# Performance work log

Measured on AMD Instinct MI355X. Metric: run time of the kernel, lower is better.

## Reference

```python
import jax, jax.numpy as jnp
import numpy as np

N_NODES = 100_000
N_EDGES = 1_600_000
B = 2
CH_N = 8; CH_E = 8; CH_K = 8; HID = 16
DT = 1.0
MAX_VALUE = 1e6


def _mlp(x, w1, b1, w2, b2):
    return jnp.tanh(x @ w1 + b1) @ w2 + b2


def _soft_clamp(x):
    return MAX_VALUE * jnp.tanh(x / MAX_VALUE)


def _seg_attn(logit, msg, seg, n):
    # logit [E], msg [E,C]; softmax over edges sharing a segment, weighted sum.
    mx = jax.ops.segment_max(logit, seg, num_segments=n)
    ex = jnp.exp(logit - mx[seg])
    den = jax.ops.segment_sum(ex, seg, num_segments=n)
    num = jax.ops.segment_sum(ex[:, None] * msg, seg, num_segments=n)
    return num / (den[:, None] + 1e-10)


def setup_inputs() -> dict:
    key = jax.random.key(0)
    ks = jax.random.split(key, 20)
    r = lambda k, shp, sc=0.3: (jax.random.normal(k, shp, dtype=jnp.float32) * sc)
    inp = {
        "nodes": jax.random.normal(ks[0], (B, N_NODES, CH_N), dtype=jnp.float32),
        "edges": jax.random.normal(ks[1], (B, N_EDGES, CH_E), dtype=jnp.float32),
        "msg_w1": r(ks[2], (2 * CH_N + CH_E, HID)),
        "msg_b1": jnp.zeros((HID,), jnp.float32),
        "msg_w2": r(ks[3], (HID, 2 * CH_N + CH_E)),
        "msg_b2": jnp.zeros((2 * CH_N + CH_E,), jnp.float32),
        "att_w1": r(ks[4], (CH_N, HID)),
        "att_b1": jnp.zeros((HID,), jnp.float32),
        "att_w2": r(ks[5], (HID, 4 * CH_K)),
        "att_b2": jnp.zeros((4 * CH_K,), jnp.float32),
        "upd_w1": r(ks[6], (3 * CH_N, HID)),
        "upd_b1": jnp.zeros((HID,), jnp.float32),
        "upd_w2": r(ks[7], (HID, CH_N)),
        "upd_b2": jnp.zeros((CH_N,), jnp.float32),
        "sources": jax.random.randint(ks[8], (N_EDGES,), 0, N_NODES, dtype=jnp.int32).astype(jnp.int64) if False else jax.random.randint(ks[8], (N_EDGES,), 0, N_NODES),
        "targets": jax.random.randint(ks[9], (N_EDGES,), 0, N_NODES),
    }
    return inp


def reference(nodes, edges, msg_w1, msg_b1, msg_w2, msg_b2,
              att_w1, att_b1, att_w2, att_b2,
              upd_w1, upd_b1, upd_w2, upd_b2,
              sources, targets):
    # --- per-edge messages: gather endpoint nodes, concat with edge state ---
    m_x = jnp.concatenate([nodes[:, sources], nodes[:, targets], edges], axis=2)  # [B,E,2*ch_n+ch_e]
    m = _mlp(m_x, msg_w1, msg_b1, msg_w2, msg_b2)
    m_a = m[..., :CH_N]                 # message to source node
    m_b = m[..., CH_N:2 * CH_N]         # message to target node
    m_ab = m[..., 2 * CH_N:]            # edge update

    # --- attention keys/queries per node (4*ch_k) ---
    att = _mlp(nodes, att_w1, att_b1, att_w2, att_b2)  # [B,N,4*ch_k]
    a_key, a_query, b_key, b_query = jnp.split(att, 4, axis=2)
    scale = 1.0 / np.sqrt(CH_K).astype(np.float32)
    logit_a = (a_query[:, sources] * b_key[:, targets]).sum(-1) * scale  # [B,E]
    logit_b = (b_query[:, targets] * a_key[:, sources]).sum(-1) * scale

    agg_a = jax.vmap(lambda l, ms: _seg_attn(l, ms, sources, N_NODES))(logit_a, m_a)  # [B,N,ch_n]
    agg_b = jax.vmap(lambda l, ms: _seg_attn(l, ms, targets, N_NODES))(logit_b, m_b)

    # --- node update ---
    u_x = jnp.concatenate([nodes, agg_a, agg_b], axis=2)  # [B,N,3*ch_n]
    upd = _mlp(u_x, upd_w1, upd_b1, upd_w2, upd_b2)

    new_nodes = _soft_clamp(nodes + DT * upd)
    new_edges = _soft_clamp(edges + DT * m_ab)
    return new_nodes, new_edges
```

## Files before the change

### kernel.cpp

```cpp
#include <hip/hip_runtime.h>

#define NN 100000
#define NE 1600000
#define NB 2
#define CH 8
#define HID 16
#define NTILES 98

typedef unsigned int uint;
typedef float f32x4 __attribute__((ext_vector_type(4)));

__device__ __forceinline__ float soft_clamp(float x) {
    float y = x * 1e-6f;
    return x * (1.0f - 0.33333333f * y * y);
}
__device__ __forceinline__ float fast_tanh(float x) {
    float ax = fabsf(x);
    float t = __expf(-2.0f * ax);
    float r = (1.0f - t) / (1.0f + t);
    return copysignf(r, x);
}
__device__ __forceinline__ void load8(const float* __restrict__ p, float* x) {
    float4 a = ((const float4*)p)[0];
    float4 b = ((const float4*)p)[1];
    x[0]=a.x; x[1]=a.y; x[2]=a.z; x[3]=a.w; x[4]=b.x; x[5]=b.y; x[6]=b.z; x[7]=b.w;
}
__device__ __forceinline__ void store8(float* __restrict__ p, const float* x) {
    ((float4*)p)[0] = make_float4(x[0],x[1],x[2],x[3]);
    ((float4*)p)[1] = make_float4(x[4],x[5],x[6],x[7]);
}
__device__ __forceinline__ void f4w(float* p, float4 v){ p[0]=v.x; p[1]=v.y; p[2]=v.z; p[3]=v.w; }

__device__ __forceinline__ uint bfu(float x) {
    uint u = __float_as_uint(x);
    return (u + 0x7fffu + ((u >> 16) & 1u)) >> 16;
}
__device__ __forceinline__ float ubf(uint u) { return __uint_as_float(u << 16); }

__device__ __forceinline__ ushort f2h(float x) {
    _Float16 h = (_Float16)x;
    union { _Float16 h; ushort u; } c; c.h = h; return c.u;
}
__device__ __forceinline__ float h2f(uint u) {
    union { ushort u; _Float16 h; } c; c.u = (ushort)u; return (float)c.h;
}
__device__ __forceinline__ float dot8h(uint4 a, uint4 b) {
    const uint* pa = &a.x; const uint* pb = &b.x;
    float s = 0.0f;
#pragma unroll
    for (int i = 0; i < 4; i++) {
        s += h2f(pa[i] & 0xffffu) * h2f(pb[i] & 0xffffu);
        s += h2f(pa[i] >> 16)     * h2f(pb[i] >> 16);
    }
    return s;
}

__device__ __forceinline__ void acc8(float* h, uint4 v, const float* __restrict__ w) {
    const uint* p = &v.x;
#pragma unroll
    for (int i = 0; i < 4; i++) {
        float x0 = h2f(p[i] & 0xffffu), x1 = h2f(p[i] >> 16);
#pragma unroll
        for (int j = 0; j < HID; j++) h[j] += x0 * w[(2*i)*HID + j];
#pragma unroll
        for (int j = 0; j < HID; j++) h[j] += x1 * w[(2*i+1)*HID + j];
    }
}

__device__ __forceinline__ void dot_pair(const float* __restrict__ h,
                                         const float* __restrict__ sw2,
                                         const float* __restrict__ sb2,
                                         int kp, float& a0, float& a1) {
    a0 = sb2[2*kp]; a1 = sb2[2*kp+1];
#pragma unroll
    for (int j = 0; j < HID; j++) {
        a0 += h[j] * sw2[j*24 + 2*kp];
        a1 += h[j] * sw2[j*24 + 2*kp + 1];
    }
}

__global__ void __launch_bounds__(256)
att_pack_kernel(const float* __restrict__ nodes,
                const float* __restrict__ w1, const float* __restrict__ b1,
                const float* __restrict__ w2, const float* __restrict__ b2,
                uint4* __restrict__ S, uint4* __restrict__ T,
                float4* __restrict__ nodesP,
                int* __restrict__ cntA, int* __restrict__ cntB) {
    __shared__ float sw1[CH*HID], sb1[HID], sw2[HID*32], sb2[32];
    int tid = threadIdx.x;
    for (int i = tid; i < CH*HID; i += 256) sw1[i] = w1[i];
    for (int i = tid; i < HID; i += 256) sb1[i] = b1[i];
    for (int i = tid; i < HID*32; i += 256) sw2[i] = w2[i];
    for (int i = tid; i < 32; i += 256) sb2[i] = b2[i];
    __syncthreads();
    int n = blockIdx.x * 256 + tid;
    if (n >= NN) return;
    int b = blockIdx.y;
    size_t base = (size_t)b * NN + n;

    if (b == 0) { cntA[n] = 0; cntB[n] = 0; }

    float x[CH];
    load8(nodes + base * CH, x);
    nodesP[(size_t)n*4 + b*2]     = make_float4(x[0],x[1],x[2],x[3]);
    nodesP[(size_t)n*4 + b*2 + 1] = make_float4(x[4],x[5],x[6],x[7]);

    float h[HID];
#pragma unroll
    for (int j = 0; j < HID; j++) {
        float acc = sb1[j];
#pragma unroll
        for (int i = 0; i < CH; i++) acc += x[i] * sw1[i*HID + j];
        h[j] = fast_tanh(acc);
    }
    float o[32];
#pragma unroll
    for (int k = 0; k < 32; k++) {
        float acc = sb2[k];
#pragma unroll
        for (int j = 0; j < HID; j++) acc += h[j] * sw2[j*32 + k];
        o[k] = acc;
    }
    uint4 nx, ak, aq, bk, bq;
    nx.x=f2h(x[0]) |(f2h(x[1]) <<16); nx.y=f2h(x[2]) |(f2h(x[3]) <<16);
    nx.z=f2h(x[4]) |(f2h(x[5]) <<16); nx.w=f2h(x[6]) |(f2h(x[7]) <<16);
    ak.x=f2h(o[0]) |(f2h(o[1]) <<16); ak.y=f2h(o[2]) |(f2h(o[3]) <<16);
    ak.z=f2h(o[4]) |(f2h(o[5]) <<16); ak.w=f2h(o[6]) |(f2h(o[7]) <<16);
    aq.x=f2h(o[8]) |(f2h(o[9]) <<16); aq.y=f2h(o[10])|(f2h(o[11])<<16);
    aq.z=f2h(o[12])|(f2h(o[13])<<16); aq.w=f2h(o[14])|(f2h(o[15])<<16);
    bk.x=f2h(o[16])|(f2h(o[17])<<16); bk.y=f2h(o[18])|(f2h(o[19])<<16);
    bk.z=f2h(o[20])|(f2h(o[21])<<16); bk.w=f2h(o[22])|(f2h(o[23])<<16);
    bq.x=f2h(o[24])|(f2h(o[25])<<16); bq.y=f2h(o[26])|(f2h(o[27])<<16);
    bq.z=f2h(o[28])|(f2h(o[29])<<16); bq.w=f2h(o[30])|(f2h(o[31])<<16);
    size_t sl = (size_t)n*8 + b*4;
    S[sl+0] = nx; S[sl+1] = ak; S[sl+2] = aq;
    T[sl+0] = nx; T[sl+1] = bk; T[sl+2] = bq;
}

__global__ void __launch_bounds__(256)
hist_rank_kernel(const int* __restrict__ src, const int* __restrict__ tgt,
                 int* __restrict__ cntA, int* __restrict__ cntB,
                 int* __restrict__ rankA, int* __restrict__ rankB) {
    int e = blockIdx.x * 256 + threadIdx.x;
    if (e >= NE) return;
    rankA[e] = atomicAdd(&cntA[src[e]], 1);
    rankB[e] = atomicAdd(&cntB[tgt[e]], 1);
}

__global__ void __launch_bounds__(256)
scan_part_kernel(const int* __restrict__ cnt, int* __restrict__ part) {
    int y = blockIdx.y;
    const int* c = cnt + (size_t)y * NN;
    __shared__ int s[256];
    int t = threadIdx.x, bx = blockIdx.x;
    int base = bx * 1024 + t * 4;
    int sum = 0;
#pragma unroll
    for (int k = 0; k < 4; k++) { int i = base + k; sum += (i < NN) ? c[i] : 0; }
    s[t] = sum; __syncthreads();
    for (int off = 128; off > 0; off >>= 1) { if (t < off) s[t] += s[t + off]; __syncthreads(); }
    if (t == 0) part[y * 256 + bx] = s[0];
}

__global__ void __launch_bounds__(256)
scan_top_kernel(int* __restrict__ part, int* __restrict__ rowA, int* __restrict__ rowB) {
    int y = blockIdx.y; int t = threadIdx.x;
    __shared__ int s[256];
    int v = (t < NTILES) ? part[y * 256 + t] : 0;
    s[t] = v; __syncthreads();
    for (int off = 1; off < 256; off <<= 1) {
        int x = (t >= off) ? s[t - off] : 0;
        __syncthreads();
        s[t] += x;
        __syncthreads();
    }
    part[y * 256 + t] = t ? s[t - 1] : 0;
    if (t == 0) (y ? rowB : rowA)[NN] = NE;
}

__global__ void __launch_bounds__(256)
scan_down_kernel(const int* __restrict__ cnt, const int* __restrict__ part,
                 int* __restrict__ rowA, int* __restrict__ rowB) {
    int y = blockIdx.y;
    const int* c = cnt + (size_t)y * NN;
    int* row = y ? rowB : rowA;
    __shared__ int s[256];
    int t = threadIdx.x, bx = blockIdx.x;
    int base = bx * 1024 + t * 4;
    int v[4]; int tsum = 0;
#pragma unroll
    for (int k = 0; k < 4; k++) { int i = base + k; v[k] = (i < NN) ? c[i] : 0; tsum += v[k]; }
    s[t] = tsum; __syncthreads();
    for (int off = 1; off < 256; off <<= 1) {
        int x = (t >= off) ? s[t - off] : 0;
        __syncthreads();
        s[t] += x;
        __syncthreads();
    }
    int run = part[y * 256 + bx] + s[t] - tsum;
#pragma unroll
    for (int k = 0; k < 4; k++) {
        int i = base + k;
        if (i < NN) row[i] = run;
        run += v[k];
    }
}

__global__ void __launch_bounds__(256)
fill_kernel(const int* __restrict__ src, const int* __restrict__ tgt,
            const int* __restrict__ rowA, const int* __restrict__ rowB,
            const int* __restrict__ rankA, const int* __restrict__ rankB,
            int* __restrict__ eidA, int* __restrict__ eidB) {
    int e = blockIdx.x * 256 + threadIdx.x;
    if (e >= NE) return;
    eidA[rowA[src[e]] + rankA[e]] = e;
    eidB[rowB[tgt[e]] + rankB[e]] = e;
}

__global__ void __launch_bounds__(256, 2)
edge_kernel(const uint4* __restrict__ S, const uint4* __restrict__ T,
            const float* __restrict__ edges,
            const int* __restrict__ src, const int* __restrict__ tgt,
            const float* __restrict__ w1, const float* __restrict__ b1,
            const float* __restrict__ w2, const float* __restrict__ b2,
            float* __restrict__ out_edges,
            uint4* __restrict__ recA, uint4* __restrict__ recB) {
    __shared__ float sw1[24*HID], sb1[HID], sw2[HID*24], sb2[24];
    int tid = threadIdx.x;
    for (int i = tid; i < 24*HID; i += 256) sw1[i] = w1[i];
    for (int i = tid; i < HID; i += 256) sb1[i] = b1[i];
    for (int i = tid; i < HID*24; i += 256) sw2[i] = w2[i];
    for (int i = tid; i < 24; i += 256) sb2[i] = b2[i];
    __syncthreads();
    int b = blockIdx.x;
    int e = blockIdx.y * 256 + tid;
    int s = src[e], t = tgt[e];
    const float scale = 0.35355339059327373f;

    size_t sl = (size_t)s*8 + b*4, tl = (size_t)t*8 + b*4;
    uint4 sn = S[sl], ak = S[sl+1], aq = S[sl+2];
    uint4 tn = T[tl], bk = T[tl+1], bq = T[tl+2];
    f32x4 e0, e1;
    {
        const f32x4* ep = (const f32x4*)(edges + ((size_t)b*NE + e)*CH);
        e0 = __builtin_nontemporal_load(ep);
        e1 = __builtin_nontemporal_load(ep + 1);
    }

    float la = scale * dot8h(aq, bk);
    float lb = scale * dot8h(bq, ak);

    float h[HID];
#pragma unroll
    for (int j = 0; j < HID; j++) h[j] = sb1[j];
    acc8(h, sn, sw1);
    acc8(h, tn, sw1 + 8*HID);
    float ef[8];
    ef[0]=e0.x; ef[1]=e0.y; ef[2]=e0.z; ef[3]=e0.w;
    ef[4]=e1.x; ef[5]=e1.y; ef[6]=e1.z; ef[7]=e1.w;
#pragma unroll
    for (int i = 0; i < 8; i++) {
#pragma unroll
        for (int j = 0; j < HID; j++) h[j] += ef[i] * sw1[(16+i)*HID + j];
    }
#pragma unroll
    for (int j = 0; j < HID; j++) h[j] = fast_tanh(h[j]);

    uint wA[4], wB[4];
#pragma unroll
    for (int kp = 0; kp < 4; kp++) {
        float a0, a1;
        dot_pair(h, sw2, sb2, kp, a0, a1);
        wA[kp] = bfu(a0) | (bfu(a1) << 16);
    }
#pragma unroll
    for (int kp = 4; kp < 8; kp++) {
        float a0, a1;
        dot_pair(h, sw2, sb2, kp, a0, a1);
        wB[kp-4] = bfu(a0) | (bfu(a1) << 16);
    }
    f32x4 o0, o1;
    {
        float a0, a1;
        dot_pair(h, sw2, sb2, 8,  a0, a1); o0.x = soft_clamp(ef[0]+a0); o0.y = soft_clamp(ef[1]+a1);
        dot_pair(h, sw2, sb2, 9,  a0, a1); o0.z = soft_clamp(ef[2]+a0); o0.w = soft_clamp(ef[3]+a1);
        dot_pair(h, sw2, sb2, 10, a0, a1); o1.x = soft_clamp(ef[4]+a0); o1.y = soft_clamp(ef[5]+a1);
        dot_pair(h, sw2, sb2, 11, a0, a1); o1.z = soft_clamp(ef[6]+a0); o1.w = soft_clamp(ef[7]+a1);
    }

    {
        f32x4* op = (f32x4*)(out_edges + ((size_t)b*NE + e)*CH);
        __builtin_nontemporal_store(o0, op);
        __builtin_nontemporal_store(o1, op + 1);
    }

    recA[(size_t)e*4 + b*2]     = make_uint4(__float_as_uint(la), wA[0], wA[1], wA[2]);
    recA[(size_t)e*4 + b*2 + 1] = make_uint4(wA[3], 0u, 0u, 0u);
    recB[(size_t)e*4 + b*2]     = make_uint4(__float_as_uint(lb), wB[0], wB[1], wB[2]);
    recB[(size_t)e*4 + b*2 + 1] = make_uint4(wB[3], 0u, 0u, 0u);
}

__device__ __forceinline__ void aggregate1(int beg, int end, const int* __restrict__ eid,
                                           const uint4* __restrict__ rec, int boff,
                                           float* __restrict__ o) {
    float mx = -1e30f, den = 0.0f, num[CH];
#pragma unroll
    for (int c = 0; c < CH; c++) num[c] = 0.0f;
    for (int i = beg; i < end; ++i) {
        int e = eid[i];
        const uint4* P = rec + (size_t)e*4 + boff;
        uint4 q0 = P[0], q1 = P[1];
        float l = __uint_as_float(q0.x);
        float nm = fmaxf(mx, l);
        float r = __expf(mx - nm), w = __expf(l - nm);
        mx = nm; den = den * r + w;
        float mm[CH];
        mm[0]=ubf(q0.y&0xffffu); mm[1]=ubf(q0.y>>16);
        mm[2]=ubf(q0.z&0xffffu); mm[3]=ubf(q0.z>>16);
        mm[4]=ubf(q0.w&0xffffu); mm[5]=ubf(q0.w>>16);
        mm[6]=ubf(q1.x&0xffffu); mm[7]=ubf(q1.x>>16);
#pragma unroll
        for (int c = 0; c < CH; c++) num[c] = num[c] * r + w * mm[c];
    }
    float inv = 1.0f / (den + 1e-10f);
#pragma unroll
    for (int c = 0; c < CH; c++) o[c] = num[c] * inv;
}

__global__ void __launch_bounds__(256)
node_kernel(const float4* __restrict__ nodesP,
            const int* __restrict__ rowA, const int* __restrict__ rowB,
            const int* __restrict__ eidA, const int* __restrict__ eidB,
            const uint4* __restrict__ recA, const uint4* __restrict__ recB,
            const float* __restrict__ w1, const float* __restrict__ b1,
            const float* __restrict__ w2, const float* __restrict__ b2,
            float* __restrict__ out_nodes) {
    __shared__ float sw1[24*HID], sb1[HID], sw2[HID*CH], sb2[CH];
    int tid = threadIdx.x;
    for (int i = tid; i < 24*HID; i += 256) sw1[i] = w1[i];
    for (int i = tid; i < HID; i += 256) sb1[i] = b1[i];
    for (int i = tid; i < HID*CH; i += 256) sw2[i] = w2[i];
    for (int i = tid; i < CH; i += 256) sb2[i] = b2[i];
    __syncthreads();
    int g = blockIdx.x * 256 + tid;
    int n = g >> 1, b = g & 1;
    if (n >= NN) return;

    float in[24];
    float4 np0 = nodesP[(size_t)n*4 + b*2], np1 = nodesP[(size_t)n*4 + b*2 + 1];
    f4w(in, np0); f4w(in + 4, np1);

    aggregate1(rowA[n], rowA[n+1], eidA, recA, b*2, in + 8);
    aggregate1(rowB[n], rowB[n+1], eidB, recB, b*2, in + 16);

    float h[HID];
#pragma unroll
    for (int j = 0; j < HID; j++) {
        float acc = sb1[j];
#pragma unroll
        for (int i = 0; i < 24; i++) acc += in[i] * sw1[i*HID + j];
        h[j] = fast_tanh(acc);
    }
    float no[CH];
#pragma unroll
    for (int k = 0; k < CH; k++) {
        float acc = sb2[k];
#pragma unroll
        for (int j = 0; j < HID; j++) acc += h[j] * sw2[j*CH + k];
        no[k] = soft_clamp(in[k] + acc);
    }
    store8(out_nodes + ((size_t)b*NN + n)*CH, no);
}

extern "C" void kernel_launch(void* const* d_in, const int* in_sizes, int n_in,
                              void* d_out, int out_size, void* d_ws, size_t ws_size,
                              hipStream_t stream) {
    const float* nodes  = (const float*)d_in[0];
    const float* edges  = (const float*)d_in[1];
    const float* msg_w1 = (const float*)d_in[2];
    const float* msg_b1 = (const float*)d_in[3];
    const float* msg_w2 = (const float*)d_in[4];
    const float* msg_b2 = (const float*)d_in[5];
    const float* att_w1 = (const float*)d_in[6];
    const float* att_b1 = (const float*)d_in[7];
    const float* att_w2 = (const float*)d_in[8];
    const float* att_b2 = (const float*)d_in[9];
    const float* upd_w1 = (const float*)d_in[10];
    const float* upd_b1 = (const float*)d_in[11];
    const float* upd_w2 = (const float*)d_in[12];
    const float* upd_b2 = (const float*)d_in[13];
    const int*   sources = (const int*)d_in[14];
    const int*   targets = (const int*)d_in[15];

    float* out       = (float*)d_out;
    float* out_nodes = out;
    float* out_edges = out + (size_t)NB * NN * CH;

    char* wp = (char*)d_ws;
    size_t off = 0;
    auto take = [&](size_t bytes) -> char* {
        char* p = wp + off;
        off = (off + bytes + 255) & ~(size_t)255;
        return p;
    };
    uint4*  S      = (uint4*)take((size_t)NN * NB * 64);
    uint4*  T      = (uint4*)take((size_t)NN * NB * 64);
    float4* nodesP = (float4*)take((size_t)NN * 64);
    int*    cnt    = (int*)take((size_t)2 * NN * 4);
    int*    rowA   = (int*)take((size_t)(NN + 1) * 4);
    int*    rowB   = (int*)take((size_t)(NN + 1) * 4);
    int*    part   = (int*)take((size_t)2 * 256 * 4);
    int*    rankA  = (int*)take((size_t)NE * 4);
    int*    rankB  = (int*)take((size_t)NE * 4);
    int*    eidA   = (int*)take((size_t)NE * 4);
    int*    eidB   = (int*)take((size_t)NE * 4);
    uint4*  recA   = (uint4*)take((size_t)NE * 64);
    uint4*  recB   = (uint4*)take((size_t)NE * 64);
    int* cntA = cnt, *cntB = cnt + NN;

    dim3 gn((NN + 255) / 256, NB);
    dim3 gn2((2*NN + 255) / 256);
    dim3 ge1((NE + 255) / 256);
    dim3 geb(NB, NE / 256);
    dim3 gs(NTILES, 2);
    dim3 gt(1, 2);

    att_pack_kernel<<<gn, 256, 0, stream>>>(nodes, att_w1, att_b1, att_w2, att_b2,
                                            S, T, nodesP, cntA, cntB);
    hist_rank_kernel<<<ge1, 256, 0, stream>>>(sources, targets, cntA, cntB, rankA, rankB);
    scan_part_kernel<<<gs, 256, 0, stream>>>(cnt, part);
    scan_top_kernel<<<gt, 256, 0, stream>>>(part, rowA, rowB);
    scan_down_kernel<<<gs, 256, 0, stream>>>(cnt, part, rowA, rowB);
    fill_kernel<<<ge1, 256, 0, stream>>>(sources, targets, rowA, rowB, rankA, rankB,
                                         eidA, eidB);
    edge_kernel<<<geb, 256, 0, stream>>>(S, T, edges, sources, targets,
                                         msg_w1, msg_b1, msg_w2, msg_b2,
                                         out_edges, recA, recB);
    node_kernel<<<gn2, 256, 0, stream>>>(nodesP, rowA, rowB, eidA, eidB, recA, recB,
                                         upd_w1, upd_b1, upd_w2, upd_b2, out_nodes);
}
```

Baseline: 549.3 us.

## Process two edges per thread and interleave both node aggregation streams

The edge kernel now handles two edges per thread and issues all gather loads for both before computing, which raises memory-level parallelism for the random node-table gathers. The grid is halved to match. The node kernel merges the A and B online-softmax aggregation loops into one loop that advances both lists together, so two independent dependent-load chains are in flight at once. The cost is higher register pressure in the edge kernel, which may reduce occupancy, and extra branching in the merged loop.

```diff
diff --git a/kernel.cpp b/kernel.cpp
--- a/kernel.cpp
+++ b/kernel.cpp
@@ -217,6 +217,59 @@
     eidB[rowB[tgt[e]] + rankB[e]] = e;
 }
 
+__device__ __forceinline__ void edge_proc(int b, int e, uint4 sn, uint4 tn,
+                                          f32x4 ed0, f32x4 ed1, float la, float lb,
+                                          const float* sw1, const float* sb1,
+                                          const float* sw2, const float* sb2,
+                                          float* __restrict__ out_edges,
+                                          uint4* __restrict__ recA, uint4* __restrict__ recB) {
+    float h[HID];
+#pragma unroll
+    for (int j = 0; j < HID; j++) h[j] = sb1[j];
+    acc8(h, sn, sw1);
+    acc8(h, tn, sw1 + 8*HID);
+    float ef[8];
+    ef[0]=ed0.x; ef[1]=ed0.y; ef[2]=ed0.z; ef[3]=ed0.w;
+    ef[4]=ed1.x; ef[5]=ed1.y; ef[6]=ed1.z; ef[7]=ed1.w;
+#pragma unroll
+    for (int i = 0; i < 8; i++) {
+#pragma unroll
+        for (int j = 0; j < HID; j++) h[j] += ef[i] * sw1[(16+i)*HID + j];
+    }
+#pragma unroll
+    for (int j = 0; j < HID; j++) h[j] = fast_tanh(h[j]);
+
+    uint wA[4], wB[4];
+#pragma unroll
+    for (int kp = 0; kp < 4; kp++) {
+        float a0, a1;
+        dot_pair(h, sw2, sb2, kp, a0, a1);
+        wA[kp] = bfu(a0) | (bfu(a1) << 16);
+    }
+#pragma unroll
+    for (int kp = 4; kp < 8; kp++) {
+        float a0, a1;
+        dot_pair(h, sw2, sb2, kp, a0, a1);
+        wB[kp-4] = bfu(a0) | (bfu(a1) << 16);
+    }
+    f32x4 o0, o1;
+    {
+        float a0, a1;
+        dot_pair(h, sw2, sb2, 8,  a0, a1); o0.x = soft_clamp(ef[0]+a0); o0.y = soft_clamp(ef[1]+a1);
+        dot_pair(h, sw2, sb2, 9,  a0, a1); o0.z = soft_clamp(ef[2]+a0); o0.w = soft_clamp(ef[3]+a1);
+        dot_pair(h, sw2, sb2, 10, a0, a1); o1.x = soft_clamp(ef[4]+a0); o1.y = soft_clamp(ef[5]+a1);
+        dot_pair(h, sw2, sb2, 11, a0, a1); o1.z = soft_clamp(ef[6]+a0); o1.w = soft_clamp(ef[7]+a1);
+    }
+    f32x4* op = (f32x4*)(out_edges + ((size_t)b*NE + e)*CH);
+    __builtin_nontemporal_store(o0, op);
+    __builtin_nontemporal_store(o1, op + 1);
+
+    recA[(size_t)e*4 + b*2]     = make_uint4(__float_as_uint(la), wA[0], wA[1], wA[2]);
+    recA[(size_t)e*4 + b*2 + 1] = make_uint4(wA[3], 0u, 0u, 0u);
+    recB[(size_t)e*4 + b*2]     = make_uint4(__float_as_uint(lb), wB[0], wB[1], wB[2]);
+    recB[(size_t)e*4 + b*2 + 1] = make_uint4(wB[3], 0u, 0u, 0u);
+}
+
 __global__ void __launch_bounds__(256, 2)
 edge_kernel(const uint4* __restrict__ S, const uint4* __restrict__ T,
             const float* __restrict__ edges,
@@ -233,98 +286,35 @@
     for (int i = tid; i < 24; i += 256) sb2[i] = b2[i];
     __syncthreads();
     int b = blockIdx.x;
-    int e = blockIdx.y * 256 + tid;
-    int s = src[e], t = tgt[e];
+    int e1 = blockIdx.y * 512 + tid;
+    int e2 = e1 + 256;
+    int s1 = src[e1], t1 = tgt[e1];
+    int s2 = src[e2], t2 = tgt[e2];
     const float scale = 0.35355339059327373f;
 
-    size_t sl = (size_t)s*8 + b*4, tl = (size_t)t*8 + b*4;
-    uint4 sn = S[sl], ak = S[sl+1], aq = S[sl+2];
-    uint4 tn = T[tl], bk = T[tl+1], bq = T[tl+2];
-    f32x4 e0, e1;
+    size_t sl1 = (size_t)s1*8 + b*4, tl1 = (size_t)t1*8 + b*4;
+    size_t sl2 = (size_t)s2*8 + b*4, tl2 = (size_t)t2*8 + b*4;
+    uint4 sn1 = S[sl1], ak1 = S[sl1+1], aq1 = S[sl1+2];
+    uint4 tn1 = T[tl1], bk1 = T[tl1+1], bq1 = T[tl1+2];
+    uint4 sn2 = S[sl2], ak2 = S[sl2+1], aq2 = S[sl2+2];
+    uint4 tn2 = T[tl2], bk2 = T[tl2+1], bq2 = T[tl2+2];
+    f32x4 e10, e11, e20, e21;
     {
-        const f32x4* ep = (const f32x4*)(edges + ((size_t)b*NE + e)*CH);
-        e0 = __builtin_nontemporal_load(ep);
-        e1 = __builtin_nontemporal_load(ep + 1);
-    }
-
-    float la = scale * dot8h(aq, bk);
-    float lb = scale * dot8h(bq, ak);
-
-    float h[HID];
-#pragma unroll
-    for (int j = 0; j < HID; j++) h[j] = sb1[j];
-    acc8(h, sn, sw1);
-    acc8(h, tn, sw1 + 8*HID);
-    float ef[8];
-    ef[0]=e0.x; ef[1]=e0.y; ef[2]=e0.z; ef[3]=e0.w;
-    ef[4]=e1.x; ef[5]=e1.y; ef[6]=e1.z; ef[7]=e1.w;
-#pragma unroll
-    for (int i = 0; i < 8; i++) {
-#pragma unroll
-        for (int j = 0; j < HID; j++) h[j] += ef[i] * sw1[(16+i)*HID + j];
-    }
-#pragma unroll
-    for (int j = 0; j < HID; j++) h[j] = fast_tanh(h[j]);
-
-    uint wA[4], wB[4];
-#pragma unroll
-    for (int kp = 0; kp < 4; kp++) {
-        float a0, a1;
-        dot_pair(h, sw2, sb2, kp, a0, a1);
-        wA[kp] = bfu(a0) | (bfu(a1) << 16);
-    }
-#pragma unroll
-    for (int kp = 4; kp < 8; kp++) {
-        float a0, a1;
-        dot_pair(h, sw2, sb2, kp, a0, a1);
-        wB[kp-4] = bfu(a0) | (bfu(a1) << 16);
-    }
-    f32x4 o0, o1;
-    {
-        float a0, a1;
-        dot_pair(h, sw2, sb2, 8,  a0, a1); o0.x = soft_clamp(ef[0]+a0); o0.y = soft_clamp(ef[1]+a1);
-        dot_pair(h, sw2, sb2, 9,  a0, a1); o0.z = soft_clamp(ef[2]+a0); o0.w = soft_clamp(ef[3]+a1);
-        dot_pair(h, sw2, sb2, 10, a0, a1); o1.x = soft_clamp(ef[4]+a0); o1.y = soft_clamp(ef[5]+a1);
-        dot_pair(h, sw2, sb2, 11, a0, a1); o1.z = soft_clamp(ef[6]+a0); o1.w = soft_clamp(ef[7]+a1);
-    }
-
-    {
-        f32x4* op = (f32x4*)(out_edges + ((size_t)b*NE + e)*CH);
-        __builtin_nontemporal_store(o0, op);
-        __builtin_nontemporal_store(o1, op + 1);
-    }
-
-    recA[(size_t)e*4 + b*2]     = make_uint4(__float_as_uint(la), wA[0], wA[1], wA[2]);
-    recA[(size_t)e*4 + b*2 + 1] = make_uint4(wA[3], 0u, 0u, 0u);
-    recB[(size_t)e*4 + b*2]     = make_uint4(__float_as_uint(lb), wB[0], wB[1], wB[2]);
-    recB[(size_t)e*4 + b*2 + 1] = make_uint4(wB[3], 0u, 0u, 0u);
-}
-
-__device__ __forceinline__ void aggregate1(int beg, int end, const int* __restrict__ eid,
-                                           const uint4* __restrict__ rec, int boff,
-                                           float* __restrict__ o) {
-    float mx = -1e30f, den = 0.0f, num[CH];
-#pragma unroll
-    for (int c = 0; c < CH; c++) num[c] = 0.0f;
-    for (int i = beg; i < end; ++i) {
-        int e = eid[i];
-        const uint4* P = rec + (size_t)e*4 + boff;
-        uint4 q0 = P[0], q1 = P[1];
-        float l = __uint_as_float(q0.x);
-        float nm = fmaxf(mx, l);
-        float r = __expf(mx - nm), w = __expf(l - nm);
-        mx = nm; den = den * r + w;
-        float mm[CH];
-        mm[0]=ubf(q0.y&0xffffu); mm[1]=ubf(q0.y>>16);
-        mm[2]=ubf(q0.z&0xffffu); mm[3]=ubf(q0.z>>16);
-        mm[4]=ubf(q0.w&0xffffu); mm[5]=ubf(q0.w>>16);
-        mm[6]=ubf(q1.x&0xffffu); mm[7]=ubf(q1.x>>16);
-#pragma unroll
-        for (int c = 0; c < CH; c++) num[c] = num[c] * r + w * mm[c];
-    }
-    float inv = 1.0f / (den + 1e-10f);
-#pragma unroll
-    for (int c = 0; c < CH; c++) o[c] = num[c] * inv;
+        const f32x4* ep1 = (const f32x4*)(edges + ((size_t)b*NE + e1)*CH);
+        const f32x4* ep2 = (const f32x4*)(edges + ((size_t)b*NE + e2)*CH);
+        e10 = __builtin_nontemporal_load(ep1);
+        e11 = __builtin_nontemporal_load(ep1 + 1);
+        e20 = __builtin_nontemporal_load(ep2);
+        e21 = __builtin_nontemporal_load(ep2 + 1);
+    }
+
+    float la1 = scale * dot8h(aq1, bk1), lb1 = scale * dot8h(bq1, ak1);
+    float la2 = scale * dot8h(aq2, bk2), lb2 = scale * dot8h(bq2, ak2);
+
+    edge_proc(b, e1, sn1, tn1, e10, e11, la1, lb1, sw1, sb1, sw2, sb2,
+              out_edges, recA, recB);
+    edge_proc(b, e2, sn2, tn2, e20, e21, la2, lb2, sw1, sb1, sw2, sb2,
+              out_edges, recA, recB);
 }
 
 __global__ void __launch_bounds__(256)
@@ -345,13 +335,57 @@
     int g = blockIdx.x * 256 + tid;
     int n = g >> 1, b = g & 1;
     if (n >= NN) return;
+    int boff = b*2;
+
+    int iA = rowA[n], endA = rowA[n+1];
+    int iB = rowB[n], endB = rowB[n+1];
+
+    float mxA = -1e30f, denA = 0.0f, numA[CH];
+    float mxB = -1e30f, denB = 0.0f, numB[CH];
+#pragma unroll
+    for (int c = 0; c < CH; c++) { numA[c] = 0.0f; numB[c] = 0.0f; }
+
+    while (iA < endA || iB < endB) {
+        if (iA < endA) {
+            int e = eidA[iA++];
+            const uint4* P = recA + (size_t)e*4 + boff;
+            uint4 q0 = P[0], q1 = P[1];
+            float l = __uint_as_float(q0.x);
+            float nm = fmaxf(mxA, l);
+            float r = __expf(mxA - nm), w = __expf(l - nm);
+            mxA = nm; denA = denA * r + w;
+            float mm[CH];
+            mm[0]=ubf(q0.y&0xffffu); mm[1]=ubf(q0.y>>16);
+            mm[2]=ubf(q0.z&0xffffu); mm[3]=ubf(q0.z>>16);
+            mm[4]=ubf(q0.w&0xffffu); mm[5]=ubf(q0.w>>16);
+            mm[6]=ubf(q1.x&0xffffu); mm[7]=ubf(q1.x>>16);
+#pragma unroll
+            for (int c = 0; c < CH; c++) numA[c] = numA[c] * r + w * mm[c];
+        }
+        if (iB < endB) {
+            int e = eidB[iB++];
+            const uint4* P = recB + (size_t)e*4 + boff;
+            uint4 q0 = P[0], q1 = P[1];
+            float l = __uint_as_float(q0.x);
+            float nm = fmaxf(mxB, l);
+            float r = __expf(mxB - nm), w = __expf(l - nm);
+            mxB = nm; denB = denB * r + w;
+            float mm[CH];
+            mm[0]=ubf(q0.y&0xffffu); mm[1]=ubf(q0.y>>16);
+            mm[2]=ubf(q0.z&0xffffu); mm[3]=ubf(q0.z>>16);
+            mm[4]=ubf(q0.w&0xffffu); mm[5]=ubf(q0.w>>16);
+            mm[6]=ubf(q1.x&0xffffu); mm[7]=ubf(q1.x>>16);
+#pragma unroll
+            for (int c = 0; c < CH; c++) numB[c] = numB[c] * r + w * mm[c];
+        }
+    }
 
     float in[24];
     float4 np0 = nodesP[(size_t)n*4 + b*2], np1 = nodesP[(size_t)n*4 + b*2 + 1];
     f4w(in, np0); f4w(in + 4, np1);
-
-    aggregate1(rowA[n], rowA[n+1], eidA, recA, b*2, in + 8);
-    aggregate1(rowB[n], rowB[n+1], eidB, recB, b*2, in + 16);
+    float invA = 1.0f / (denA + 1e-10f), invB = 1.0f / (denB + 1e-10f);
+#pragma unroll
+    for (int c = 0; c < CH; c++) { in[8+c] = numA[c] * invA; in[16+c] = numB[c] * invB; }
 
     float h[HID];
 #pragma unroll
@@ -421,7 +455,7 @@
     dim3 gn((NN + 255) / 256, NB);
     dim3 gn2((2*NN + 255) / 256);
     dim3 ge1((NE + 255) / 256);
-    dim3 geb(NB, NE / 256);
+    dim3 geb(NB, NE / 512);
     dim3 gs(NTILES, 2);
     dim3 gt(1, 2);
 
```

Result: slower. 1.604 ms (+192.1%).
